# Optimization experiments

Hardware: AMD Instinct MI355X
Metric: run time of the kernel (lower is better)

The kernel has to match this reference:

```python
import jax, jax.numpy as jnp
import numpy as np

B, T, H, A = 64, 512, 1024, 300


def setup_inputs() -> dict:
    key = jax.random.key(0)
    ks = jax.random.split(key, 12)
    s = 0.02  # weight init scale
    return {
        "hidden": jax.random.normal(ks[0], (B, T, H), jnp.float32),
        "aspect": jax.random.normal(ks[1], (B, 1, A), jnp.float32),
        # torch Linear stores weight as [out_features, in_features]
        "W_h": jax.random.normal(ks[2], (H, H), jnp.float32) * s,
        "b_h": jax.random.normal(ks[3], (H,), jnp.float32) * s,
        "W_v": jax.random.normal(ks[4], (A, A), jnp.float32) * s,
        "b_v": jax.random.normal(ks[5], (A,), jnp.float32) * s,
        "w_w": jax.random.normal(ks[6], (1, H + A), jnp.float32) * s,
        "w_b": jax.random.normal(ks[7], (1,), jnp.float32) * s,
        "W_p": jax.random.normal(ks[8], (H, H), jnp.float32) * s,
        "b_p": jax.random.normal(ks[9], (H,), jnp.float32) * s,
        "W_x": jax.random.normal(ks[10], (H, H), jnp.float32) * s,
        "b_x": jax.random.normal(ks[11], (H,), jnp.float32) * s,
    }


def reference(hidden, aspect, W_h, b_h, W_v, b_v, w_w, w_b, W_p, b_p, W_x, b_x):
    # transformed aspect: [B, 1, A], repeated along seq dim -> [B, T, A]
    tv = aspect @ W_v.T + b_v
    rep_v = jnp.broadcast_to(tv, (hidden.shape[0], hidden.shape[1], tv.shape[-1]))
    # M = tanh(concat(W_h(hidden), repeated_v)) : [B, T, H+A]
    M = jnp.tanh(jnp.concatenate([hidden @ W_h.T + b_h, rep_v], axis=-1))
    # additive attention scores -> softmax over T
    scores = jnp.einsum("bts,os->bto", M, w_w)[..., 0] + w_b[0]  # [B, T]
    alpha = jax.nn.softmax(scores, axis=-1)
    # weighted sum r = alpha^T @ hidden : [B, 1, H]
    r = jnp.einsum("bt,bth->bh", alpha, hidden)[:, None, :]
    # NOTE: faithful to original torch broadcasting quirk:
    # [B,1,H] + [B,H] broadcasts to [B,B,H]
    output = jnp.tanh((r @ W_p.T + b_p) + (hidden[:, -1, :] @ W_x.T + b_x))
    return output
```

## Files before the change

### kernel.cpp

```cpp
#include <hip/hip_runtime.h>
#include <hip/hip_bf16.h>
#include <stdint.h>

#define B_DIM 64
#define T_DIM 512
#define H_DIM 1024
#define K_DIM 1024
#define M_DIM (B_DIM * T_DIM)

typedef __bf16 bf16x8 __attribute__((ext_vector_type(8)));
typedef float f32x4 __attribute__((ext_vector_type(4)));

__device__ __forceinline__ float tanh_fast(float x) {
  float e = __expf(2.0f * x);
  return 1.0f - 2.0f / (e + 1.0f);
}

__device__ __forceinline__ float bf2f(unsigned short u) {
  return __uint_as_float(((unsigned int)u) << 16);
}

__device__ __forceinline__ void async_cp16(const void* gp, void* lp) {
  __builtin_amdgcn_global_load_lds(
      reinterpret_cast<const __attribute__((address_space(1))) uint32_t*>(
          reinterpret_cast<uintptr_t>(gp)),
      reinterpret_cast<__attribute__((address_space(3))) uint32_t*>(
          reinterpret_cast<uintptr_t>(lp)),
      16, 0, 0);
}

__global__ void prep_kernel(const float* __restrict__ hidden, __bf16* __restrict__ hidBf,
                            const float* __restrict__ Wh, __bf16* __restrict__ whBf,
                            float* __restrict__ scores) {
  const int bid = blockIdx.x, tid = threadIdx.x;
  if (bid < 32768) {
    int i = bid * 256 + tid;
    float4 v = reinterpret_cast<const float4*>(hidden)[i];
    union { __bf16 b[4]; uint2 u; } o;
    o.b[0] = (__bf16)v.x; o.b[1] = (__bf16)v.y; o.b[2] = (__bf16)v.z; o.b[3] = (__bf16)v.w;
    reinterpret_cast<uint2*>(hidBf)[i] = o.u;
  } else if (bid < 33792) {
    int i = (bid - 32768) * 256 + tid;
    float4 v = reinterpret_cast<const float4*>(Wh)[i];
    union { __bf16 b[4]; uint2 u; } o;
    o.b[0] = (__bf16)v.x; o.b[1] = (__bf16)v.y; o.b[2] = (__bf16)v.z; o.b[3] = (__bf16)v.w;
    reinterpret_cast<uint2*>(whBf)[i] = o.u;
  } else {
    int i = (bid - 33792) * 256 + tid;
    reinterpret_cast<float4*>(scores)[i] = make_float4(0.f, 0.f, 0.f, 0.f);
  }
}

#define GM_BK 64
__global__ __launch_bounds__(256, 2) void gemm_scores_kernel(
    const __bf16* __restrict__ A, const __bf16* __restrict__ Bm,
    const float* __restrict__ bh, const float* __restrict__ ww,
    float* __restrict__ scores) {
  __shared__ __attribute__((aligned(16))) __bf16 lA[256 * GM_BK];
  __shared__ __attribute__((aligned(16))) __bf16 lB[128 * GM_BK];

  const int tid = threadIdx.x;
  const int bid = blockIdx.x;
  const int m0 = (bid & 127) * 256;
  const int n0 = (bid >> 7) * 128;

  const int wv = tid >> 6;
  const int lane = tid & 63;
  const int wm = wv & 1, wn = wv >> 1;
  const int r16 = lane & 15, quad = lane >> 4;

  f32x4 acc[8][4] = {};

  const __bf16* gA[8]; __bf16* lAd[8];
#pragma unroll
  for (int j = 0; j < 8; ++j) {
    int c = j * 256 + tid;
    int row = c >> 3;
    int p = c & 7;
    int kc = p ^ ((row >> 1) & 7);
    gA[j] = A + (size_t)(m0 + row) * K_DIM + kc * 8;
    lAd[j] = &lA[c * 8];
  }
  const __bf16* gB[4]; __bf16* lBd[4];
#pragma unroll
  for (int j = 0; j < 4; ++j) {
    int c = j * 256 + tid;
    int row = c >> 3;
    int p = c & 7;
    int kc = p ^ ((row >> 1) & 7);
    gB[j] = Bm + (size_t)(n0 + row) * K_DIM + kc * 8;
    lBd[j] = &lB[c * 8];
  }

  const int sw = r16 >> 1;
  const __bf16* pa[2]; const __bf16* pb[2];
#pragma unroll
  for (int kk = 0; kk < 2; ++kk) {
    pa[kk] = &lA[(wm * 128 + r16) * GM_BK + ((kk * 4 + quad) ^ sw) * 8];
    pb[kk] = &lB[(wn * 64 + r16) * GM_BK + ((kk * 4 + quad) ^ sw) * 8];
  }

#pragma unroll
  for (int k0 = 0; k0 < K_DIM; k0 += GM_BK) {
#pragma unroll
    for (int j = 0; j < 8; ++j) async_cp16(gA[j] + k0, lAd[j]);
#pragma unroll
    for (int j = 0; j < 4; ++j) async_cp16(gB[j] + k0, lBd[j]);
    __syncthreads();
#pragma unroll
    for (int kk = 0; kk < 2; ++kk) {
      bf16x8 bfr[4];
#pragma unroll
      for (int ni = 0; ni < 4; ++ni)
        bfr[ni] = *reinterpret_cast<const bf16x8*>(pb[kk] + ni * 16 * GM_BK);
      bf16x8 af[8];
#pragma unroll
      for (int mi = 0; mi < 8; ++mi)
        af[mi] = *reinterpret_cast<const bf16x8*>(pa[kk] + mi * 16 * GM_BK);
#pragma unroll
      for (int mi = 0; mi < 8; ++mi)
#pragma unroll
        for (int ni = 0; ni < 4; ++ni)
          acc[mi][ni] = __builtin_amdgcn_mfma_f32_16x16x32_bf16(af[mi], bfr[ni], acc[mi][ni], 0, 0, 0);
    }
    __syncthreads();
  }

  float bhv[4], wwv[4];
#pragma unroll
  for (int ni = 0; ni < 4; ++ni) {
    int n = n0 + wn * 64 + ni * 16 + r16;
    bhv[ni] = bh[n];
    wwv[ni] = ww[n];
  }
#pragma unroll
  for (int mi = 0; mi < 8; ++mi) {
#pragma unroll
    for (int rg = 0; rg < 4; ++rg) {
      float s = 0.f;
#pragma unroll
      for (int ni = 0; ni < 4; ++ni)
        s += tanh_fast(acc[mi][ni][rg] + bhv[ni]) * wwv[ni];
      s += __shfl_xor(s, 1, 16);
      s += __shfl_xor(s, 2, 16);
      s += __shfl_xor(s, 4, 16);
      s += __shfl_xor(s, 8, 16);
      if (r16 == 0) {
        int m = m0 + wm * 128 + mi * 16 + quad * 4 + rg;
        atomicAdd(&scores[m], s);
      }
    }
  }
}

__global__ void wsum_kernel(const float* __restrict__ scores,
                            const __bf16* __restrict__ hiddenBf,
                            float* __restrict__ r8) {
  __shared__ float al[64];
  __shared__ float red[8];
  const int bid = blockIdx.x, tid = threadIdx.x;
  const int b = bid >> 3, tc = bid & 7;
  const int wv = tid >> 6, lane = tid & 63;
  float v0 = scores[b * T_DIM + tid];
  float v1 = scores[b * T_DIM + 256 + tid];
  float mx = fmaxf(v0, v1);
#pragma unroll
  for (int off = 1; off < 64; off <<= 1) mx = fmaxf(mx, __shfl_xor(mx, off, 64));
  if (lane == 0) red[wv] = mx;
  __syncthreads();
  mx = fmaxf(fmaxf(red[0], red[1]), fmaxf(red[2], red[3]));
  float e0 = __expf(v0 - mx), e1 = __expf(v1 - mx);
  float s = e0 + e1;
#pragma unroll
  for (int off = 1; off < 64; off <<= 1) s += __shfl_xor(s, off, 64);
  if (lane == 0) red[4 + wv] = s;
  __syncthreads();
  float inv = 1.0f / (red[4] + red[5] + red[6] + red[7]);
  if (tid < 64) al[tid] = __expf(scores[b * T_DIM + tc * 64 + tid] - mx) * inv;
  __syncthreads();
  const __bf16* hp = hiddenBf + (size_t)b * T_DIM * H_DIM + (size_t)tc * 64 * H_DIM + tid * 4;
  float4 acc = make_float4(0.f, 0.f, 0.f, 0.f);
#pragma unroll 8
  for (int t = 0; t < 64; ++t) {
    float a = al[t];
    ushort4 u = *reinterpret_cast<const ushort4*>(hp + (size_t)t * H_DIM);
    acc.x += a * bf2f(u.x);
    acc.y += a * bf2f(u.y);
    acc.z += a * bf2f(u.z);
    acc.w += a * bf2f(u.w);
  }
  *reinterpret_cast<float4*>(r8 + (size_t)(b * 8 + tc) * H_DIM + tid * 4) = acc;
}

#define IG 4
__global__ void rowvec2_kernel(const float* __restrict__ r8,
                               const float* __restrict__ hidden,
                               const float* __restrict__ W_p, const float* __restrict__ b_p,
                               const float* __restrict__ W_x, const float* __restrict__ b_x,
                               float* __restrict__ rp, float* __restrict__ xq) {
  __shared__ __attribute__((aligned(16))) float sv[IG][H_DIM];
  const int h0 = blockIdx.x * 64;
  const int i0 = blockIdx.y * IG;
  const int which = blockIdx.z;
  const int tid = threadIdx.x;
  const float* W = which ? W_x : W_p;
  const float* bias = which ? b_x : b_p;
  float* dst = which ? xq : rp;
  if (which == 0) {
#pragma unroll
    for (int ii = 0; ii < IG; ++ii) {
      const float* src = r8 + (size_t)(i0 + ii) * 8 * H_DIM + tid * 4;
      float4 a = *reinterpret_cast<const float4*>(src);
#pragma unroll
      for (int tc = 1; tc < 8; ++tc) {
        float4 v = *reinterpret_cast<const float4*>(src + (size_t)tc * H_DIM);
        a.x += v.x; a.y += v.y; a.z += v.z; a.w += v.w;
      }
      *reinterpret_cast<float4*>(&sv[ii][tid * 4]) = a;
    }
  } else {
#pragma unroll
    for (int ii = 0; ii < IG; ++ii) {
      const float* src = hidden + (size_t)(i0 + ii) * T_DIM * H_DIM +
                         (size_t)(T_DIM - 1) * H_DIM + tid * 4;
      *reinterpret_cast<float4*>(&sv[ii][tid * 4]) = *reinterpret_cast<const float4*>(src);
    }
  }
  __syncthreads();
  const int hl = tid >> 2;
  const int kq = tid & 3;
  const float* wr = W + (size_t)(h0 + hl) * H_DIM + kq * 4;
  float acc[IG] = {};
#pragma unroll 8
  for (int j = 0; j < 64; ++j) {
    float4 w4 = *reinterpret_cast<const float4*>(wr + j * 16);
#pragma unroll
    for (int ii = 0; ii < IG; ++ii) {
      float4 s4 = *reinterpret_cast<const float4*>(&sv[ii][kq * 4 + j * 16]);
      acc[ii] += w4.x * s4.x + w4.y * s4.y + w4.z * s4.z + w4.w * s4.w;
    }
  }
#pragma unroll
  for (int ii = 0; ii < IG; ++ii) {
    acc[ii] += __shfl_xor(acc[ii], 1, 4);
    acc[ii] += __shfl_xor(acc[ii], 2, 4);
  }
  if (kq == 0) {
    float bb = bias[h0 + hl];
#pragma unroll
    for (int ii = 0; ii < IG; ++ii)
      dst[(size_t)(i0 + ii) * H_DIM + h0 + hl] = acc[ii] + bb;
  }
}

__global__ void final_kernel(const float* __restrict__ rp, const float* __restrict__ xq,
                             float* __restrict__ out) {
  int idx = blockIdx.x * 256 + threadIdx.x;
  int e = idx * 4;
  int i = e >> 16;
  int j = (e >> 10) & 63;
  int h = e & 1023;
  float4 a = *reinterpret_cast<const float4*>(&rp[i * H_DIM + h]);
  float4 b = *reinterpret_cast<const float4*>(&xq[j * H_DIM + h]);
  float4 o;
  o.x = tanh_fast(a.x + b.x);
  o.y = tanh_fast(a.y + b.y);
  o.z = tanh_fast(a.z + b.z);
  o.w = tanh_fast(a.w + b.w);
  *reinterpret_cast<float4*>(&out[e]) = o;
}

extern "C" void kernel_launch(void* const* d_in, const int* in_sizes, int n_in,
                              void* d_out, int out_size, void* d_ws, size_t ws_size,
                              hipStream_t stream) {
  const float* hidden = (const float*)d_in[0];
  const float* W_h = (const float*)d_in[2];
  const float* b_h = (const float*)d_in[3];
  const float* w_w = (const float*)d_in[6];
  const float* W_p = (const float*)d_in[8];
  const float* b_p = (const float*)d_in[9];
  const float* W_x = (const float*)d_in[10];
  const float* b_x = (const float*)d_in[11];
  float* out = (float*)d_out;

  char* ws = (char*)d_ws;
  __bf16* hidBf = (__bf16*)ws;
  __bf16* whBf = (__bf16*)(ws + 67108864);
  float* r8 = (float*)(ws + 67108864);
  float* scores = (float*)(ws + 69206016);
  float* rpB = (float*)(ws + 69337088);
  float* xqB = (float*)(ws + 69599232);

  prep_kernel<<<33824, 256, 0, stream>>>(hidden, hidBf, W_h, whBf, scores);

  gemm_scores_kernel<<<1024, 256, 0, stream>>>(hidBf, whBf, b_h, w_w, scores);

  wsum_kernel<<<512, 256, 0, stream>>>(scores, hidBf, r8);

  rowvec2_kernel<<<dim3(H_DIM / 64, B_DIM / IG, 2), 256, 0, stream>>>(
      r8, hidden, W_p, b_p, W_x, b_x, rpB, xqB);

  final_kernel<<<(B_DIM * B_DIM * H_DIM / 4) / 256, 256, 0, stream>>>(rpB, xqB, out);
}
```

Baseline: 344.3 us.

## Replace score atomics with per-tile partial buffers and use grid-stride prep/final kernels

The GEMM epilogue now reduces each N-tile's scores in LDS and writes one partial per N-tile to a buffer, instead of doing atomicAdd into a zeroed scores array. This removes the score zero-initialisation from the prep kernel. The softmax/weighted-sum kernel sums the eight partials and caches the scores in shared memory. The prep and final kernels become grid-stride loops with 2048 blocks. The GEMM is split into two launches over halves of M. The rp/xq buffers are moved into the dead hidden-bf16 workspace region. The trade-offs are an extra kernel launch, a larger partial-score buffer and more reads in the wsum kernel.

```diff
diff --git a/kernel.cpp b/kernel.cpp
--- a/kernel.cpp
+++ b/kernel.cpp
@@ -7,6 +7,8 @@
 #define H_DIM 1024
 #define K_DIM 1024
 #define M_DIM (B_DIM * T_DIM)
+#define GM_BK 64
+#define IG 4
 
 typedef __bf16 bf16x8 __attribute__((ext_vector_type(8)));
 typedef float f32x4 __attribute__((ext_vector_type(4)));
@@ -29,48 +31,43 @@
       16, 0, 0);
 }
 
+__device__ __forceinline__ void cvt4(const float4& v, uint2* dst) {
+  union { __bf16 b[4]; uint2 u; } o;
+  o.b[0] = (__bf16)v.x; o.b[1] = (__bf16)v.y; o.b[2] = (__bf16)v.z; o.b[3] = (__bf16)v.w;
+  *dst = o.u;
+}
+
+#define STRIDE_NTHR (2048 * 256)
 __global__ void prep_kernel(const float* __restrict__ hidden, __bf16* __restrict__ hidBf,
-                            const float* __restrict__ Wh, __bf16* __restrict__ whBf,
-                            float* __restrict__ scores) {
-  const int bid = blockIdx.x, tid = threadIdx.x;
-  if (bid < 32768) {
-    int i = bid * 256 + tid;
-    float4 v = reinterpret_cast<const float4*>(hidden)[i];
-    union { __bf16 b[4]; uint2 u; } o;
-    o.b[0] = (__bf16)v.x; o.b[1] = (__bf16)v.y; o.b[2] = (__bf16)v.z; o.b[3] = (__bf16)v.w;
-    reinterpret_cast<uint2*>(hidBf)[i] = o.u;
-  } else if (bid < 33792) {
-    int i = (bid - 32768) * 256 + tid;
-    float4 v = reinterpret_cast<const float4*>(Wh)[i];
-    union { __bf16 b[4]; uint2 u; } o;
-    o.b[0] = (__bf16)v.x; o.b[1] = (__bf16)v.y; o.b[2] = (__bf16)v.z; o.b[3] = (__bf16)v.w;
-    reinterpret_cast<uint2*>(whBf)[i] = o.u;
-  } else {
-    int i = (bid - 33792) * 256 + tid;
-    reinterpret_cast<float4*>(scores)[i] = make_float4(0.f, 0.f, 0.f, 0.f);
-  }
-}
-
-#define GM_BK 64
+                            const float* __restrict__ Wh, __bf16* __restrict__ whBf) {
+  const int gt = blockIdx.x * 256 + threadIdx.x;
+  const float4* hs = reinterpret_cast<const float4*>(hidden);
+  uint2* hd = reinterpret_cast<uint2*>(hidBf);
+#pragma unroll 4
+  for (int i = gt; i < 8388608; i += STRIDE_NTHR) {
+    cvt4(hs[i], &hd[i]);
+  }
+  const float4* wsrc = reinterpret_cast<const float4*>(Wh);
+  uint2* wd = reinterpret_cast<uint2*>(whBf);
+  if (gt < 262144) cvt4(wsrc[gt], &wd[gt]);
+}
+
 __global__ __launch_bounds__(256, 2) void gemm_scores_kernel(
     const __bf16* __restrict__ A, const __bf16* __restrict__ Bm,
     const float* __restrict__ bh, const float* __restrict__ ww,
-    float* __restrict__ scores) {
+    float* __restrict__ scoresP, int m_base) {
   __shared__ __attribute__((aligned(16))) __bf16 lA[256 * GM_BK];
   __shared__ __attribute__((aligned(16))) __bf16 lB[128 * GM_BK];
-
   const int tid = threadIdx.x;
   const int bid = blockIdx.x;
-  const int m0 = (bid & 127) * 256;
-  const int n0 = (bid >> 7) * 128;
-
+  const int m0 = (bid & 63) * 256 + m_base;
+  const int nIdx = bid >> 6;
+  const int n0 = nIdx * 128;
   const int wv = tid >> 6;
   const int lane = tid & 63;
   const int wm = wv & 1, wn = wv >> 1;
   const int r16 = lane & 15, quad = lane >> 4;
-
   f32x4 acc[8][4] = {};
-
   const __bf16* gA[8]; __bf16* lAd[8];
 #pragma unroll
   for (int j = 0; j < 8; ++j) {
@@ -91,7 +88,6 @@
     gB[j] = Bm + (size_t)(n0 + row) * K_DIM + kc * 8;
     lBd[j] = &lB[c * 8];
   }
-
   const int sw = r16 >> 1;
   const __bf16* pa[2]; const __bf16* pb[2];
 #pragma unroll
@@ -99,7 +95,6 @@
     pa[kk] = &lA[(wm * 128 + r16) * GM_BK + ((kk * 4 + quad) ^ sw) * 8];
     pb[kk] = &lB[(wn * 64 + r16) * GM_BK + ((kk * 4 + quad) ^ sw) * 8];
   }
-
 #pragma unroll
   for (int k0 = 0; k0 < K_DIM; k0 += GM_BK) {
 #pragma unroll
@@ -125,7 +120,7 @@
     }
     __syncthreads();
   }
-
+  float* sBuf = reinterpret_cast<float*>(lA);
   float bhv[4], wwv[4];
 #pragma unroll
   for (int ni = 0; ni < 4; ++ni) {
@@ -146,23 +141,32 @@
       s += __shfl_xor(s, 4, 16);
       s += __shfl_xor(s, 8, 16);
       if (r16 == 0) {
-        int m = m0 + wm * 128 + mi * 16 + quad * 4 + rg;
-        atomicAdd(&scores[m], s);
+        int lm = wm * 128 + mi * 16 + quad * 4 + rg;
+        sBuf[wn * 256 + lm] = s;
       }
     }
   }
-}
-
-__global__ void wsum_kernel(const float* __restrict__ scores,
+  __syncthreads();
+  scoresP[nIdx * M_DIM + m0 + tid] = sBuf[tid] + sBuf[256 + tid];
+}
+
+__global__ void wsum_kernel(const float* __restrict__ scoresP,
                             const __bf16* __restrict__ hiddenBf,
                             float* __restrict__ r8) {
+  __shared__ float sc[512];
   __shared__ float al[64];
   __shared__ float red[8];
   const int bid = blockIdx.x, tid = threadIdx.x;
   const int b = bid >> 3, tc = bid & 7;
   const int wv = tid >> 6, lane = tid & 63;
-  float v0 = scores[b * T_DIM + tid];
-  float v1 = scores[b * T_DIM + 256 + tid];
+  float v0 = 0.f, v1 = 0.f;
+#pragma unroll
+  for (int p = 0; p < 8; ++p) {
+    v0 += scoresP[p * M_DIM + b * T_DIM + tid];
+    v1 += scoresP[p * M_DIM + b * T_DIM + 256 + tid];
+  }
+  sc[tid] = v0;
+  sc[tid + 256] = v1;
   float mx = fmaxf(v0, v1);
 #pragma unroll
   for (int off = 1; off < 64; off <<= 1) mx = fmaxf(mx, __shfl_xor(mx, off, 64));
@@ -176,7 +180,7 @@
   if (lane == 0) red[4 + wv] = s;
   __syncthreads();
   float inv = 1.0f / (red[4] + red[5] + red[6] + red[7]);
-  if (tid < 64) al[tid] = __expf(scores[b * T_DIM + tc * 64 + tid] - mx) * inv;
+  if (tid < 64) al[tid] = __expf(sc[tc * 64 + tid] - mx) * inv;
   __syncthreads();
   const __bf16* hp = hiddenBf + (size_t)b * T_DIM * H_DIM + (size_t)tc * 64 * H_DIM + tid * 4;
   float4 acc = make_float4(0.f, 0.f, 0.f, 0.f);
@@ -192,7 +196,6 @@
   *reinterpret_cast<float4*>(r8 + (size_t)(b * 8 + tc) * H_DIM + tid * 4) = acc;
 }
 
-#define IG 4
 __global__ void rowvec2_kernel(const float* __restrict__ r8,
                                const float* __restrict__ hidden,
                                const float* __restrict__ W_p, const float* __restrict__ b_p,
@@ -255,19 +258,22 @@
 
 __global__ void final_kernel(const float* __restrict__ rp, const float* __restrict__ xq,
                              float* __restrict__ out) {
-  int idx = blockIdx.x * 256 + threadIdx.x;
-  int e = idx * 4;
-  int i = e >> 16;
-  int j = (e >> 10) & 63;
-  int h = e & 1023;
-  float4 a = *reinterpret_cast<const float4*>(&rp[i * H_DIM + h]);
-  float4 b = *reinterpret_cast<const float4*>(&xq[j * H_DIM + h]);
-  float4 o;
-  o.x = tanh_fast(a.x + b.x);
-  o.y = tanh_fast(a.y + b.y);
-  o.z = tanh_fast(a.z + b.z);
-  o.w = tanh_fast(a.w + b.w);
-  *reinterpret_cast<float4*>(&out[e]) = o;
+  const int gt = blockIdx.x * 256 + threadIdx.x;
+#pragma unroll
+  for (int idx = gt; idx < 1048576; idx += STRIDE_NTHR) {
+    int e = idx * 4;
+    int i = e >> 16;
+    int j = (e >> 10) & 63;
+    int h = e & 1023;
+    float4 a = *reinterpret_cast<const float4*>(&rp[i * H_DIM + h]);
+    float4 b = *reinterpret_cast<const float4*>(&xq[j * H_DIM + h]);
+    float4 o;
+    o.x = tanh_fast(a.x + b.x);
+    o.y = tanh_fast(a.y + b.y);
+    o.z = tanh_fast(a.z + b.z);
+    o.w = tanh_fast(a.w + b.w);
+    *reinterpret_cast<float4*>(&out[e]) = o;
+  }
 }
 
 extern "C" void kernel_launch(void* const* d_in, const int* in_sizes, int n_in,
@@ -287,18 +293,19 @@
   __bf16* hidBf = (__bf16*)ws;
   __bf16* whBf = (__bf16*)(ws + 67108864);
   float* r8 = (float*)(ws + 67108864);
-  float* scores = (float*)(ws + 69206016);
-  float* rpB = (float*)(ws + 69337088);
-  float* xqB = (float*)(ws + 69599232);
-
-  prep_kernel<<<33824, 256, 0, stream>>>(hidden, hidBf, W_h, whBf, scores);
-
-  gemm_scores_kernel<<<1024, 256, 0, stream>>>(hidBf, whBf, b_h, w_w, scores);
-
-  wsum_kernel<<<512, 256, 0, stream>>>(scores, hidBf, r8);
+  float* scoresP = (float*)(ws + 69206016);
+  float* rpB = (float*)ws;
+  float* xqB = (float*)(ws + 262144);
+
+  prep_kernel<<<2048, 256, 0, stream>>>(hidden, hidBf, W_h, whBf);
+
+  gemm_scores_kernel<<<512, 256, 0, stream>>>(hidBf, whBf, b_h, w_w, scoresP, 0);
+  gemm_scores_kernel<<<512, 256, 0, stream>>>(hidBf, whBf, b_h, w_w, scoresP, 16384);
+
+  wsum_kernel<<<512, 256, 0, stream>>>(scoresP, hidBf, r8);
 
   rowvec2_kernel<<<dim3(H_DIM / 64, B_DIM / IG, 2), 256, 0, stream>>>(
       r8, hidden, W_p, b_p, W_x, b_x, rpB, xqB);
 
-  final_kernel<<<(B_DIM * B_DIM * H_DIM / 4) / 256, 256, 0, stream>>>(rpB, xqB, out);
-}
+  final_kernel<<<2048, 256, 0, stream>>>(rpB, xqB, out);
+}
```

New measurement: 354.2 us. +2.9%, slower.
